# Optimization experiments

Hardware: AMD Instinct MI355X
Metric: run time of the kernel (lower is better)

Reference implementation:

```python
import jax, jax.numpy as jnp
import numpy as np

B, N, HID = 4, 16384, 512
H, M = 8, 32          # num_heads, num_slices
D = HID // H          # head_dim = 64


def setup_inputs() -> dict:
    key = jax.random.key(0)
    ks = jax.random.split(key, 8)
    std = 0.02
    return {
        "x": jax.random.normal(ks[0], (B, N, HID), jnp.float32),
        # Linear weights stored as [in, out] (y = x @ W + b)
        "wkv_w": jax.random.normal(ks[1], (HID, 2 * HID), jnp.float32) * std,
        "wkv_b": jnp.zeros((2 * HID,), jnp.float32),
        "wtq": jax.random.normal(ks[2], (H, M, D), jnp.float32) * std,
        "alpha": jnp.ones((H,), jnp.float32),
        "qkv_w": jax.random.normal(ks[3], (HID, 3 * HID), jnp.float32) * std,
        "out_w": jax.random.normal(ks[4], (HID, HID), jnp.float32) * std,
        "out_b": jnp.zeros((HID,), jnp.float32),
    }


def _split_heads(t):  # [b, n, h*d] -> [b, h, n, d]
    b, n, _ = t.shape
    return t.reshape(b, n, H, D).transpose(0, 2, 1, 3)


def _mha(q, k, v):
    scale = q.shape[-1] ** -0.5
    dots = jnp.einsum('bhqd,bhkd->bhqk', q, k) * scale
    attn = jax.nn.softmax(dots, axis=-1)
    out = jnp.einsum('bhqk,bhkd->bhqd', attn, v)
    return out, attn


def reference(x, wkv_w, wkv_b, wtq, alpha, qkv_w, out_w, out_b):
    kv = x @ wkv_w + wkv_b                      # [b, n, 2*hid]
    xk, xv = kv[..., :HID], kv[..., HID:]
    xk = _split_heads(xk)                       # [b, h, n, d]
    xv = _split_heads(xv)

    # slot/slice cross-attention: softmax over the slice axis m (axis=-2)
    slice_scores = jnp.einsum('hmd,bhnd->bhmn', wtq, xk)
    slice_weights = jax.nn.softmax(slice_scores * alpha[None, :, None, None], axis=-2)
    slice_token = jnp.einsum('bhmn,bhnd->bhmd', slice_weights, xv)
    slice_token = slice_token / (slice_weights.sum(axis=-1, keepdims=True) + 1e-5)
    slice_token = slice_token.transpose(0, 2, 1, 3).reshape(B, M, HID)  # b m (h d)

    # small inner MHA over the m=32 slices
    qkv = slice_token @ qkv_w                   # [b, m, 3*hid]
    q_t = _split_heads(qkv[..., :HID])
    k_t = _split_heads(qkv[..., HID:2 * HID])
    v_t = _split_heads(qkv[..., 2 * HID:])
    out_token, attn_weights = _mha(q_t, k_t, v_t)

    # scatter slice outputs back to n positions
    out = jnp.einsum('bhmd,bhmn->bhnd', out_token, slice_weights)
    out = out.transpose(0, 2, 1, 3).reshape(B, N, HID)  # b n (h d)
    out = out @ out_w + out_b
    return out, slice_weights, alpha, jnp.zeros((H, M), jnp.float32), attn_weights
```

## Files before the change

kernel.cpp:

```cpp
#include <hip/hip_runtime.h>

#define B_ 4
#define N_ 16384
#define HID_ 512
#define H_ 8
#define M_ 32
#define D_ 64

typedef __attribute__((ext_vector_type(8))) short short8;
typedef __attribute__((ext_vector_type(4))) float f32x4;

__device__ __forceinline__ short f2bf(float f) {
    unsigned u = __float_as_uint(f);
    u += 0x7fffu + ((u >> 16) & 1u);
    return (short)(u >> 16);
}
__device__ __forceinline__ float bf2f(short s) {
    return __uint_as_float(((unsigned)(unsigned short)s) << 16);
}
__device__ __forceinline__ unsigned pack2(float a, float b) {
    return (unsigned)(unsigned short)f2bf(a) | ((unsigned)(unsigned short)f2bf(b) << 16);
}
__device__ __forceinline__ void gl_lds16(const short* g, short* l) {
    __builtin_amdgcn_global_load_lds((const __attribute__((address_space(1))) unsigned*)g,
                                     (__attribute__((address_space(3))) unsigned*)l, 16, 0, 0);
}

__global__ void k_misc(const float* __restrict__ alpha, float* __restrict__ a_out,
                       float* __restrict__ z_out, const float* __restrict__ wtq,
                       short* __restrict__ wtq_bf) {
    int i = blockIdx.x * 256 + threadIdx.x;
    wtq_bf[i] = f2bf(wtq[i]);
    if (blockIdx.x == 0) {
        int t = threadIdx.x;
        if (t < H_) a_out[t] = alpha[t];
        z_out[t] = 0.f;
    }
}

__global__ void k_cvt(const float* __restrict__ src, short* __restrict__ dst) {
    int i = blockIdx.x * 256 + threadIdx.x;
    const f32x4* s = (const f32x4*)(src) + (size_t)i * 2;
    f32x4 a = s[0], b = s[1];
    short8 o;
    o[0] = f2bf(a[0]); o[1] = f2bf(a[1]); o[2] = f2bf(a[2]); o[3] = f2bf(a[3]);
    o[4] = f2bf(b[0]); o[5] = f2bf(b[1]); o[6] = f2bf(b[2]); o[7] = f2bf(b[3]);
    ((short8*)dst)[i] = o;
}

__global__ __launch_bounds__(256)
void k_wt(const float* __restrict__ w, short* __restrict__ wt) {
    __shared__ float ls[64][65];
    const int t = threadIdx.x;
    const int n0 = blockIdx.x * 64, k0 = blockIdx.y * 64;
#pragma unroll
    for (int p = 0; p < 16; ++p) {
        int idx = p * 256 + t;
        int kk = idx >> 6, nn = idx & 63;
        ls[kk][nn] = w[(size_t)(k0 + kk) * 1024 + n0 + nn];
    }
    __syncthreads();
#pragma unroll
    for (int p = 0; p < 16; ++p) {
        int idx = p * 256 + t;
        int nn = idx >> 6, kk = idx & 63;
        wt[(size_t)(n0 + nn) * 512 + k0 + kk] = f2bf(ls[kk][nn]);
    }
}

template <bool OUT_BF16>
__global__ __launch_bounds__(256, 2)
void mfma_gemm(const short* __restrict__ A, const short* __restrict__ Bt,
               const float* __restrict__ bias, void* __restrict__ Cv,
               int K, int Ncols, int b_stride, int rows_per_b, int lgx) {
    __shared__ short As[128 * 64];
    __shared__ short Bs[128 * 64];
    const int t = threadIdx.x;
    const int nwg = gridDim.x * gridDim.y;
    int id = blockIdx.y * gridDim.x + blockIdx.x;
    id = (id & 7) * (nwg >> 3) + (id >> 3);
    const int col0 = (id & ((1 << lgx) - 1)) * 128;
    const int row0 = (id >> lgx) * 128;
    const short* Bblk = Bt;
    if (b_stride) Bblk += (size_t)(row0 / rows_per_b) * (size_t)b_stride;

    int srow[4], scol[4];
#pragma unroll
    for (int c = 0; c < 4; ++c) {
        int lin = (c * 256 + t) * 16;
        int logo = lin ^ (((lin >> 7) & 7) << 4);
        srow[c] = logo >> 7;
        scol[c] = (logo & 127) >> 1;
    }

    const int w = t >> 6;
    const int L = t & 63;
    const int wm = (w >> 1) << 6;
    const int wn = (w & 1) << 6;
    const int lm = L & 15;
    const int lq = L >> 4;

    f32x4 acc[4][4];
#pragma unroll
    for (int i = 0; i < 4; ++i)
#pragma unroll
        for (int j = 0; j < 4; ++j) acc[i][j] = (f32x4){0.f, 0.f, 0.f, 0.f};

    for (int k0 = 0; k0 < K; k0 += 64) {
#pragma unroll
        for (int c = 0; c < 4; ++c) {
            gl_lds16(A + (size_t)(row0 + srow[c]) * K + k0 + scol[c], &As[(c * 256 + t) * 8]);
            gl_lds16(Bblk + (size_t)(col0 + srow[c]) * K + k0 + scol[c], &Bs[(c * 256 + t) * 8]);
        }
        __syncthreads();
#pragma unroll
        for (int ks = 0; ks < 2; ++ks) {
            short8 af[4], bfr[4];
#pragma unroll
            for (int i = 0; i < 4; ++i) {
                const int row = wm + (i << 4) + lm;
                int pb = (row << 7) + (ks << 6) + (lq << 4);
                pb ^= (row & 7) << 4;
                af[i] = *(const short8*)&As[pb >> 1];
            }
#pragma unroll
            for (int j = 0; j < 4; ++j) {
                const int row = wn + (j << 4) + lm;
                int pb = (row << 7) + (ks << 6) + (lq << 4);
                pb ^= (row & 7) << 4;
                bfr[j] = *(const short8*)&Bs[pb >> 1];
            }
#pragma unroll
            for (int i = 0; i < 4; ++i)
#pragma unroll
                for (int j = 0; j < 4; ++j)
                    acc[i][j] = __builtin_amdgcn_mfma_f32_16x16x32_bf16(af[i], bfr[j], acc[i][j], 0, 0, 0);
        }
        __syncthreads();
    }
#pragma unroll
    for (int i = 0; i < 4; ++i) {
#pragma unroll
        for (int j = 0; j < 4; ++j) {
            const int gr = row0 + wm + (i << 4) + (lq << 2);
            const int gc = col0 + wn + (j << 4) + lm;
            const float bv = bias[gc];
#pragma unroll
            for (int r = 0; r < 4; ++r) {
                float v = acc[i][j][r] + bv;
                if constexpr (OUT_BF16)
                    ((short*)Cv)[(size_t)(gr + r) * Ncols + gc] = f2bf(v);
                else
                    ((float*)Cv)[(size_t)(gr + r) * Ncols + gc] = v;
            }
        }
    }
}

__global__ __launch_bounds__(256, 4)
void k_score(const short* __restrict__ kv, const short* __restrict__ wtq_bf,
             const float* __restrict__ alpha, float* __restrict__ sw_out,
             short* __restrict__ swT, float* __restrict__ pws) {
    __shared__ __attribute__((aligned(16))) short wT_s[M_ * 256];
    const int t = threadIdx.x;
    const int bx = blockIdx.x;
    const int chunk = bx & 63;
    const int h = (bx >> 6) & 7;
    const int b = bx >> 9;
    const int w = t >> 6;
    const int L = t & 63;
    const int lm = L & 15;
    const int g = L >> 4;
    const int n0 = chunk * 256;
    const size_t rowb = (size_t)(b * N_ + n0);
    const float al = alpha[h];

    short8 bq[2][2];
    const short* wq = wtq_bf + h * (M_ * D_);
#pragma unroll
    for (int mt = 0; mt < 2; ++mt)
#pragma unroll
        for (int ks = 0; ks < 2; ++ks)
            bq[mt][ks] = *(const short8*)(wq + (mt * 16 + lm) * 64 + ks * 32 + g * 8);

    f32x4 s[4][2];
#pragma unroll
    for (int nt = 0; nt < 4; ++nt)
#pragma unroll
        for (int mt = 0; mt < 2; ++mt) s[nt][mt] = (f32x4){0.f, 0.f, 0.f, 0.f};
#pragma unroll
    for (int ks = 0; ks < 2; ++ks) {
        short8 aq[4];
#pragma unroll
        for (int nt = 0; nt < 4; ++nt)
            aq[nt] = *(const short8*)(kv + (rowb + w * 64 + nt * 16 + lm) * 1024 +
                                      h * 64 + ks * 32 + g * 8);
        __builtin_amdgcn_s_setprio(1);
#pragma unroll
        for (int nt = 0; nt < 4; ++nt)
#pragma unroll
            for (int mt = 0; mt < 2; ++mt)
                s[nt][mt] = __builtin_amdgcn_mfma_f32_16x16x32_bf16(aq[nt], bq[mt][ks], s[nt][mt], 0, 0, 0);
        __builtin_amdgcn_s_setprio(0);
    }

#pragma unroll
    for (int nt = 0; nt < 4; ++nt)
#pragma unroll
        for (int r = 0; r < 4; ++r) {
            float v0 = s[nt][0][r] * al, v1 = s[nt][1][r] * al;
            float mx = fmaxf(v0, v1);
#pragma unroll
            for (int d2 = 1; d2 < 16; d2 <<= 1) mx = fmaxf(mx, __shfl_xor(mx, d2));
            float e0 = __expf(v0 - mx), e1 = __expf(v1 - mx);
            float sm = e0 + e1;
#pragma unroll
            for (int d2 = 1; d2 < 16; d2 <<= 1) sm += __shfl_xor(sm, d2);
            float inv = 1.f / sm;
            s[nt][0][r] = e0 * inv;
            s[nt][1][r] = e1 * inv;
        }

    float ws0 = 0.f, ws1 = 0.f;
#pragma unroll
    for (int nt = 0; nt < 4; ++nt) {
        const int nn = w * 64 + nt * 16 + g * 4;
#pragma unroll
        for (int mt = 0; mt < 2; ++mt) {
            const int m = mt * 16 + lm;
            *(f32x4*)(sw_out + ((size_t)((b * 8 + h) * 32 + m)) * N_ + n0 + nn) = s[nt][mt];
            float w4 = s[nt][mt][0] + s[nt][mt][1] + s[nt][mt][2] + s[nt][mt][3];
            if (mt == 0) ws0 += w4; else ws1 += w4;
            unsigned lo = pack2(s[nt][mt][0], s[nt][mt][1]);
            unsigned hi = pack2(s[nt][mt][2], s[nt][mt][3]);
            *(uint2*)(wT_s + m * 256 + (nn ^ ((m & 7) << 3))) = make_uint2(lo, hi);
        }
    }
    ws0 += __shfl_xor(ws0, 16); ws0 += __shfl_xor(ws0, 32);
    ws1 += __shfl_xor(ws1, 16); ws1 += __shfl_xor(ws1, 32);
    if (L < 16) {
        float* pw = pws + (((size_t)((b * 8 + h) * 64 + chunk)) * 4 + w) * 32;
        pw[lm] = ws0;
        pw[16 + lm] = ws1;
    }
    __syncthreads();

    unsigned pk[16];
#pragma unroll
    for (int mp = 0; mp < 16; ++mp) {
        unsigned a0 = (unsigned short)wT_s[(2 * mp) * 256 + (t ^ (((2 * mp) & 7) << 3))];
        unsigned a1 = (unsigned short)wT_s[(2 * mp + 1) * 256 + (t ^ (((2 * mp + 1) & 7) << 3))];
        pk[mp] = a0 | (a1 << 16);
    }
    short8* swtp = (short8*)(swT + (rowb + t) * 256 + h * 32);
#pragma unroll
    for (int q = 0; q < 4; ++q) {
        short8 v;
        v[0] = (short)(pk[4 * q] & 0xffff);     v[1] = (short)(pk[4 * q] >> 16);
        v[2] = (short)(pk[4 * q + 1] & 0xffff); v[3] = (short)(pk[4 * q + 1] >> 16);
        v[4] = (short)(pk[4 * q + 2] & 0xffff); v[5] = (short)(pk[4 * q + 2] >> 16);
        v[6] = (short)(pk[4 * q + 3] & 0xffff); v[7] = (short)(pk[4 * q + 3] >> 16);
        swtp[q] = v;
    }
}

__global__ __attribute__((amdgpu_flat_work_group_size(256, 256), amdgpu_waves_per_eu(3, 3)))
void k_wsum(const short* __restrict__ kv, const short* __restrict__ swT,
            float* __restrict__ pnum) {
    __shared__ __attribute__((aligned(16))) short wT_s[M_ * 256];
    __shared__ __attribute__((aligned(16))) short xvT_s[D_ * 256];
    const int t = threadIdx.x;
    const int bx = blockIdx.x;
    const int chunk = bx & 63;
    const int h = (bx >> 6) & 7;
    const int b = bx >> 9;
    const int w = t >> 6;
    const int L = t & 63;
    const int lm = L & 15;
    const int g = L >> 4;
    const int n0 = chunk * 256;
    const size_t rowb = (size_t)(b * N_ + n0);

    short8 xv8[8];
    const short8* xvp = (const short8*)(kv + (rowb + t) * 1024 + HID_ + h * 64);
#pragma unroll
    for (int i = 0; i < 8; ++i) xv8[i] = xvp[i];

    short8 sw4[4];
    const short8* swp = (const short8*)(swT + (rowb + t) * 256 + h * 32);
#pragma unroll
    for (int q = 0; q < 4; ++q) sw4[q] = swp[q];

#pragma unroll
    for (int q = 0; q < 4; ++q)
#pragma unroll
        for (int j = 0; j < 8; ++j) {
            const int m = q * 8 + j;
            wT_s[m * 256 + (t ^ ((m & 7) << 3))] = sw4[q][j];
        }

#pragma unroll
    for (int i = 0; i < 8; ++i)
#pragma unroll
        for (int j = 0; j < 8; ++j)
            xvT_s[(i * 8 + j) * 256 + (t ^ (j << 3))] = xv8[i][j];

    __syncthreads();

    const int dcol = w * 16 + lm;
    f32x4 acc2[2];
    acc2[0] = (f32x4){0.f, 0.f, 0.f, 0.f};
    acc2[1] = (f32x4){0.f, 0.f, 0.f, 0.f};
#pragma unroll
    for (int ks = 0; ks < 8; ++ks) {
        const int kb = ks * 32 + g * 8;
        short8 bv = *(const short8*)(xvT_s + dcol * 256 + (kb ^ ((lm & 7) << 3)));
#pragma unroll
        for (int mt = 0; mt < 2; ++mt) {
            const int m = mt * 16 + lm;
            short8 av = *(const short8*)(wT_s + m * 256 + (kb ^ ((lm & 7) << 3)));
            acc2[mt] = __builtin_amdgcn_mfma_f32_16x16x32_bf16(av, bv, acc2[mt], 0, 0, 0);
        }
    }

    float* pn = pnum + ((size_t)((b * 8 + h) * 64 + chunk)) * 2048;
#pragma unroll
    for (int mt = 0; mt < 2; ++mt)
#pragma unroll
        for (int r = 0; r < 4; ++r)
            pn[(mt * 16 + g * 4 + r) * 64 + dcol] = acc2[mt][r];
}

__global__ __launch_bounds__(256)
void k_reduce(const float* __restrict__ pnum, const float* __restrict__ pws,
              float* __restrict__ num, float* __restrict__ wsum) {
    const int bid = blockIdx.x, t = threadIdx.x;
    if (bid < 256) {
        int e = bid * 256 + t;
        int bh = e >> 11, md = e & 2047;
        const float* p = pnum + (size_t)bh * 64 * 2048 + md;
        float s = 0.f;
#pragma unroll 4
        for (int c = 0; c < 64; ++c) s += p[c * 2048];
        num[e] = s;
    } else {
        int e = (bid - 256) * 256 + t;
        int bh = e >> 5, m = e & 31;
        const float* p = pws + (size_t)bh * 64 * 4 * 32 + m;
        float s = 0.f;
#pragma unroll 4
        for (int cw = 0; cw < 256; ++cw) s += p[cw * 32];
        wsum[e] = s;
    }
}

__global__ __launch_bounds__(256, 2)
void k_qkv(const float* __restrict__ num, const float* __restrict__ wsum,
           const float* __restrict__ qkv_w, float* __restrict__ qkv) {
    __shared__ float st_s[512 * 32];
    const int t = threadIdx.x;
    const int b = blockIdx.y;
    for (int p = 0; p < 64; ++p) {
        int idx = p * 256 + t;
        int m = idx & 31, k = idx >> 5;
        int h = k >> 6, d = k & 63;
        float wsv = wsum[(b * H_ + h) * M_ + m];
        st_s[k * 32 + m] = num[((size_t)(b * H_ + h) * M_ + m) * 64 + d] / (wsv + 1e-5f);
    }
    __syncthreads();
    const int m = t >> 3;
    const int c0 = blockIdx.x * 64 + (t & 7) * 8;
    float acc[8] = {};
    for (int k = 0; k < 512; ++k) {
        float sv = st_s[k * 32 + m];
        const f32x4* wp = (const f32x4*)(qkv_w + (size_t)k * 1536 + c0);
        f32x4 w0 = wp[0], w1 = wp[1];
        acc[0] += sv * w0[0]; acc[1] += sv * w0[1]; acc[2] += sv * w0[2]; acc[3] += sv * w0[3];
        acc[4] += sv * w1[0]; acc[5] += sv * w1[1]; acc[6] += sv * w1[2]; acc[7] += sv * w1[3];
    }
    float* dst = qkv + (size_t)(b * M_ + m) * 1536 + c0;
#pragma unroll
    for (int i = 0; i < 8; ++i) dst[i] = acc[i];
}

__global__ __launch_bounds__(256)
void k_mha(const float* __restrict__ qkv, float* __restrict__ attn_out,
           float* __restrict__ ot) {
    __shared__ float q_s[32 * 65], k_s[32 * 65], v_s[32 * 65];
    __shared__ float s_s[32 * 33], p_s[32 * 33];
    const int bx = blockIdx.x;
    const int b = bx >> 3, h = bx & 7;
    const int t = threadIdx.x;
    for (int p = 0; p < 8; ++p) {
        int idx = p * 256 + t;
        int m = idx >> 6, d = idx & 63;
        size_t base = (size_t)(b * M_ + m) * 1536 + h * 64 + d;
        q_s[m * 65 + d] = qkv[base];
        k_s[m * 65 + d] = qkv[base + 512];
        v_s[m * 65 + d] = qkv[base + 1024];
    }
    __syncthreads();
    for (int p = 0; p < 4; ++p) {
        int c = p * 256 + t;
        int m = c >> 5, mm = c & 31;
        float a = 0.f;
#pragma unroll
        for (int d = 0; d < 64; ++d) a += q_s[m * 65 + d] * k_s[mm * 65 + d];
        s_s[m * 33 + mm] = a * 0.125f;
    }
    __syncthreads();
    if (t < 32) {
        float mx = -1e30f;
        for (int mm = 0; mm < 32; ++mm) mx = fmaxf(mx, s_s[t * 33 + mm]);
        float sum = 0.f;
        for (int mm = 0; mm < 32; ++mm) {
            float e = __expf(s_s[t * 33 + mm] - mx);
            p_s[t * 33 + mm] = e;
            sum += e;
        }
        float inv = 1.f / sum;
        for (int mm = 0; mm < 32; ++mm) {
            float av = p_s[t * 33 + mm] * inv;
            p_s[t * 33 + mm] = av;
            attn_out[((size_t)(b * H_ + h) * M_ + t) * M_ + mm] = av;
        }
    }
    __syncthreads();
    const int m = t >> 3, d0 = (t & 7) * 8;
    float acc[8] = {};
    for (int mm = 0; mm < 32; ++mm) {
        float av = p_s[m * 33 + mm];
#pragma unroll
        for (int j = 0; j < 8; ++j) acc[j] += av * v_s[mm * 65 + d0 + j];
    }
    float* dst = ot + ((size_t)(b * H_ + h) * M_ + m) * 64 + d0;
#pragma unroll
    for (int j = 0; j < 8; ++j) dst[j] = acc[j];
}

__global__ __launch_bounds__(256)
void k_p(const float* __restrict__ ot, const float* __restrict__ out_w,
         short* __restrict__ Pt) {
    __shared__ float ot_s[32 * 65];
    const int bh = blockIdx.y;
    const int b = bh >> 3, h = bh & 7;
    const int t = threadIdx.x;
    for (int p = 0; p < 8; ++p) {
        int idx = p * 256 + t;
        int m = idx >> 6, d = idx & 63;
        ot_s[m * 65 + d] = ot[(size_t)bh * (M_ * 64) + idx];
    }
    __syncthreads();
    const int j = blockIdx.x * 128 + (t & 127);
    const int mh = (t >> 7) * 16;
    float acc[16] = {};
    for (int d = 0; d < 64; ++d) {
        float ow = out_w[(size_t)(h * 64 + d) * HID_ + j];
#pragma unroll
        for (int i = 0; i < 16; ++i) acc[i] += ot_s[(mh + i) * 65 + d] * ow;
    }
    short* dst = Pt + ((size_t)b * HID_ + j) * (H_ * M_) + h * M_ + mh;
#pragma unroll
    for (int i = 0; i < 16; i += 2) *(unsigned*)(dst + i) = pack2(acc[i], acc[i + 1]);
}

extern "C" void kernel_launch(void* const* d_in, const int* in_sizes, int n_in,
                              void* d_out, int out_size, void* d_ws, size_t ws_size,
                              hipStream_t stream) {
    const float* x     = (const float*)d_in[0];
    const float* wkv_w = (const float*)d_in[1];
    const float* wkv_b = (const float*)d_in[2];
    const float* wtq   = (const float*)d_in[3];
    const float* alpha = (const float*)d_in[4];
    const float* qkv_w = (const float*)d_in[5];
    const float* out_w = (const float*)d_in[6];
    const float* out_b = (const float*)d_in[7];

    float* out       = (float*)d_out;
    float* sw_out    = out + (size_t)B_ * N_ * HID_;
    float* alpha_out = sw_out + (size_t)B_ * H_ * M_ * N_;
    float* zeros_out = alpha_out + H_;
    float* attn_out  = zeros_out + H_ * M_;

    short* x_bf = (short*)sw_out;
    float* pnum = out;
    float* pws  = out + 4194304;

    char* ws = (char*)d_ws;
    short* kv   = (short*)(ws);
    short* swT  = (short*)(ws + 134217728);
    short* wkvT = (short*)(ws + 167772160);
    short* Pt   = (short*)(ws + 168820736);
    float* num  = (float*)(ws + 169869312);
    float* wsum = (float*)(ws + 170131456);
    float* qkvb = (float*)(ws + 170135552);
    float* ot   = (float*)(ws + 170921984);
    short* wtq_bf = (short*)(ws + 170921984);

    k_misc<<<64, 256, 0, stream>>>(alpha, alpha_out, zeros_out, wtq, wtq_bf);
    k_cvt<<<16384, 256, 0, stream>>>(x, x_bf);
    k_wt<<<dim3(16, 8), 256, 0, stream>>>(wkv_w, wkvT);
    mfma_gemm<true><<<dim3(8, 512), 256, 0, stream>>>(
        x_bf, wkvT, wkv_b, (void*)kv, 512, 1024, 0, 1 << 30, 3);
    k_score<<<2048, 256, 0, stream>>>(kv, wtq_bf, alpha, sw_out, swT, pws);
    k_wsum<<<2048, 256, 0, stream>>>(kv, swT, pnum);
    k_reduce<<<260, 256, 0, stream>>>(pnum, pws, num, wsum);
    k_qkv<<<dim3(24, 4), 256, 0, stream>>>(num, wsum, qkv_w, qkvb);
    k_mha<<<32, 256, 0, stream>>>(qkvb, attn_out, ot);
    k_p<<<dim3(4, 32), 256, 0, stream>>>(ot, out_w, Pt);
    mfma_gemm<false><<<dim3(4, 512), 256, 0, stream>>>(
        swT, Pt, out_b, (void*)out, 256, 512, 131072, 16384, 2);
}
```

Before: 551.6 us.

## Fold slice-query weights into K projection and compute scores directly from x

Precomputes an effective weight Weff = Wk_h · wtq_h (plus an effective bias) so slice scores come from a single x @ Weff GEMM with K=512 and 256 outputs. The full 1024-wide KV projection becomes a V-only 512-wide projection, so the K half is never materialized. The change removes GEMM FLOPs and halves the kv intermediate's write and read traffic. In exchange, scores are computed from bf16 x against a bf16-rounded fused weight, which changes rounding, and a new score GEMM kernel with a softmax epilogue is added.

```diff
diff --git a/kernel.cpp b/kernel.cpp
--- a/kernel.cpp
+++ b/kernel.cpp
@@ -27,15 +27,10 @@
 }
 
 __global__ void k_misc(const float* __restrict__ alpha, float* __restrict__ a_out,
-                       float* __restrict__ z_out, const float* __restrict__ wtq,
-                       short* __restrict__ wtq_bf) {
-    int i = blockIdx.x * 256 + threadIdx.x;
-    wtq_bf[i] = f2bf(wtq[i]);
-    if (blockIdx.x == 0) {
-        int t = threadIdx.x;
-        if (t < H_) a_out[t] = alpha[t];
-        z_out[t] = 0.f;
-    }
+                       float* __restrict__ z_out) {
+    int t = threadIdx.x;
+    if (t < H_) a_out[t] = alpha[t];
+    z_out[t] = 0.f;
 }
 
 __global__ void k_cvt(const float* __restrict__ src, short* __restrict__ dst) {
@@ -52,7 +47,7 @@
 void k_wt(const float* __restrict__ w, short* __restrict__ wt) {
     __shared__ float ls[64][65];
     const int t = threadIdx.x;
-    const int n0 = blockIdx.x * 64, k0 = blockIdx.y * 64;
+    const int n0 = (blockIdx.x + 8) * 64, k0 = blockIdx.y * 64;
 #pragma unroll
     for (int p = 0; p < 16; ++p) {
         int idx = p * 256 + t;
@@ -65,6 +60,32 @@
         int idx = p * 256 + t;
         int nn = idx >> 6, kk = idx & 63;
         wt[(size_t)(n0 + nn) * 512 + k0 + kk] = f2bf(ls[kk][nn]);
+    }
+}
+
+__global__ __launch_bounds__(256)
+void k_weff(const float* __restrict__ wkv_w, const float* __restrict__ wkv_b,
+            const float* __restrict__ wtq, short* __restrict__ WeffT,
+            float* __restrict__ beff) {
+    __shared__ float wq_s[64];
+    const int c = blockIdx.x;
+    const int h = c >> 5;
+    const int t = threadIdx.x;
+    if (t < 64) wq_s[t] = wtq[c * 64 + t];
+    __syncthreads();
+#pragma unroll
+    for (int kk = 0; kk < 2; ++kk) {
+        const int k = kk * 256 + t;
+        const float* wr = wkv_w + (size_t)k * 1024 + h * 64;
+        float a = 0.f;
+#pragma unroll
+        for (int d = 0; d < 64; ++d) a += wr[d] * wq_s[d];
+        WeffT[c * 512 + k] = f2bf(a);
+    }
+    if (t == 0) {
+        float a = 0.f;
+        for (int d = 0; d < 64; ++d) a += wkv_b[h * 64 + d] * wq_s[d];
+        beff[c] = a;
     }
 }
 
@@ -157,11 +178,158 @@
     }
 }
 
-__global__ __launch_bounds__(256, 4)
-void k_score(const short* __restrict__ kv, const short* __restrict__ wtq_bf,
-             const float* __restrict__ alpha, float* __restrict__ sw_out,
-             short* __restrict__ swT, float* __restrict__ pws) {
+__global__ __launch_bounds__(256, 2)
+void k_scoreg(const short* __restrict__ A, const short* __restrict__ WeffT,
+              const float* __restrict__ beff, const float* __restrict__ alpha,
+              float* __restrict__ sw_out, short* __restrict__ swT,
+              float* __restrict__ pws) {
+    __shared__ __attribute__((aligned(16))) short smem[16384];
+    short* As = smem;
+    short* Bs = smem + 8192;
+    short* wT_s = smem;
+    const int t = threadIdx.x;
+    int id = blockIdx.y * 2 + blockIdx.x;
+    id = (id & 7) * 128 + (id >> 3);
+    const int xc = id & 1;
+    const int row0 = (id >> 1) * 128;
+    const int col0 = xc * 128;
+    const int K = 512;
+
+    int srow[4], scol[4];
+#pragma unroll
+    for (int c = 0; c < 4; ++c) {
+        int lin = (c * 256 + t) * 16;
+        int logo = lin ^ (((lin >> 7) & 7) << 4);
+        srow[c] = logo >> 7;
+        scol[c] = (logo & 127) >> 1;
+    }
+    const int w = t >> 6;
+    const int L = t & 63;
+    const int wm = (w >> 1) << 6;
+    const int wn = (w & 1) << 6;
+    const int lm = L & 15;
+    const int lq = L >> 4;
+
+    f32x4 acc[4][4];
+#pragma unroll
+    for (int i = 0; i < 4; ++i)
+#pragma unroll
+        for (int j = 0; j < 4; ++j) acc[i][j] = (f32x4){0.f, 0.f, 0.f, 0.f};
+
+    for (int k0 = 0; k0 < K; k0 += 64) {
+#pragma unroll
+        for (int c = 0; c < 4; ++c) {
+            gl_lds16(A + (size_t)(row0 + srow[c]) * K + k0 + scol[c], &As[(c * 256 + t) * 8]);
+            gl_lds16(WeffT + (size_t)(col0 + srow[c]) * K + k0 + scol[c], &Bs[(c * 256 + t) * 8]);
+        }
+        __syncthreads();
+#pragma unroll
+        for (int ks = 0; ks < 2; ++ks) {
+            short8 af[4], bfr[4];
+#pragma unroll
+            for (int i = 0; i < 4; ++i) {
+                const int row = wm + (i << 4) + lm;
+                int pb = (row << 7) + (ks << 6) + (lq << 4);
+                pb ^= (row & 7) << 4;
+                af[i] = *(const short8*)&As[pb >> 1];
+            }
+#pragma unroll
+            for (int j = 0; j < 4; ++j) {
+                const int row = wn + (j << 4) + lm;
+                int pb = (row << 7) + (ks << 6) + (lq << 4);
+                pb ^= (row & 7) << 4;
+                bfr[j] = *(const short8*)&Bs[pb >> 1];
+            }
+#pragma unroll
+            for (int i = 0; i < 4; ++i)
+#pragma unroll
+                for (int j = 0; j < 4; ++j)
+                    acc[i][j] = __builtin_amdgcn_mfma_f32_16x16x32_bf16(af[i], bfr[j], acc[i][j], 0, 0, 0);
+        }
+        __syncthreads();
+    }
+
+    const int b = row0 >> 14;
+    const int nb = row0 & 16383;
+    float be[4], alf[2];
+#pragma unroll
+    for (int j = 0; j < 4; ++j) be[j] = beff[col0 + wn + (j << 4) + lm];
+#pragma unroll
+    for (int hh = 0; hh < 2; ++hh) alf[hh] = alpha[xc * 4 + (w & 1) * 2 + hh];
+
+#pragma unroll
+    for (int i = 0; i < 4; ++i)
+#pragma unroll
+        for (int r = 0; r < 4; ++r)
+#pragma unroll
+            for (int hh = 0; hh < 2; ++hh) {
+                float v0 = (acc[i][2 * hh][r] + be[2 * hh]) * alf[hh];
+                float v1 = (acc[i][2 * hh + 1][r] + be[2 * hh + 1]) * alf[hh];
+                float mx = fmaxf(v0, v1);
+#pragma unroll
+                for (int d2 = 1; d2 < 16; d2 <<= 1) mx = fmaxf(mx, __shfl_xor(mx, d2));
+                float e0 = __expf(v0 - mx), e1 = __expf(v1 - mx);
+                float sm = e0 + e1;
+#pragma unroll
+                for (int d2 = 1; d2 < 16; d2 <<= 1) sm += __shfl_xor(sm, d2);
+                float inv = 1.f / sm;
+                acc[i][2 * hh][r] = e0 * inv;
+                acc[i][2 * hh + 1][r] = e1 * inv;
+            }
+
+    float wsj[4] = {0.f, 0.f, 0.f, 0.f};
+#pragma unroll
+    for (int i = 0; i < 4; ++i) {
+        const int tokb = wm + (i << 4) + (lq << 2);
+#pragma unroll
+        for (int j = 0; j < 4; ++j) {
+            const int h = xc * 4 + (w & 1) * 2 + (j >> 1);
+            const int m = ((j & 1) << 4) + lm;
+            f32x4 vv = acc[i][j];
+            *(f32x4*)(sw_out + ((size_t)((b * 8 + h) * 32 + m)) * N_ + nb + tokb) = vv;
+            wsj[j] += vv[0] + vv[1] + vv[2] + vv[3];
+            const int c = wn + (j << 4) + lm;
+            unsigned lo = pack2(vv[0], vv[1]);
+            unsigned hi = pack2(vv[2], vv[3]);
+            *(uint2*)(wT_s + c * 128 + (tokb ^ ((c & 7) << 3))) = make_uint2(lo, hi);
+        }
+    }
+#pragma unroll
+    for (int j = 0; j < 4; ++j) {
+        wsj[j] += __shfl_xor(wsj[j], 16);
+        wsj[j] += __shfl_xor(wsj[j], 32);
+    }
+    if (L < 16) {
+        const int panel = nb >> 7;
+#pragma unroll
+        for (int hh = 0; hh < 2; ++hh) {
+            const int h = xc * 4 + (w & 1) * 2 + hh;
+            float* pw = pws + (((size_t)((b * 8 + h) * 128 + panel)) * 2 + (w >> 1)) * 32;
+            pw[lm] = wsj[2 * hh];
+            pw[16 + lm] = wsj[2 * hh + 1];
+        }
+    }
+    __syncthreads();
+
+    const int tok = t & 127, ch = t >> 7;
+    short8* swtp = (short8*)(swT + ((size_t)(b * N_ + nb + tok)) * 256 + xc * 128 + ch * 64);
+#pragma unroll
+    for (int q = 0; q < 8; ++q) {
+        short8 v;
+#pragma unroll
+        for (int e = 0; e < 8; ++e) {
+            const int c = ch * 64 + q * 8 + e;
+            v[e] = wT_s[c * 128 + (tok ^ ((c & 7) << 3))];
+        }
+        swtp[q] = v;
+    }
+}
+
+__global__ __attribute__((amdgpu_flat_work_group_size(256, 256), amdgpu_waves_per_eu(3, 3)))
+void k_wsum(const short* __restrict__ v, const short* __restrict__ swT,
+            float* __restrict__ pnum) {
     __shared__ __attribute__((aligned(16))) short wT_s[M_ * 256];
+    __shared__ __attribute__((aligned(16))) short xvT_s[D_ * 256];
     const int t = threadIdx.x;
     const int bx = blockIdx.x;
     const int chunk = bx & 63;
@@ -173,116 +341,9 @@
     const int g = L >> 4;
     const int n0 = chunk * 256;
     const size_t rowb = (size_t)(b * N_ + n0);
-    const float al = alpha[h];
-
-    short8 bq[2][2];
-    const short* wq = wtq_bf + h * (M_ * D_);
-#pragma unroll
-    for (int mt = 0; mt < 2; ++mt)
-#pragma unroll
-        for (int ks = 0; ks < 2; ++ks)
-            bq[mt][ks] = *(const short8*)(wq + (mt * 16 + lm) * 64 + ks * 32 + g * 8);
-
-    f32x4 s[4][2];
-#pragma unroll
-    for (int nt = 0; nt < 4; ++nt)
-#pragma unroll
-        for (int mt = 0; mt < 2; ++mt) s[nt][mt] = (f32x4){0.f, 0.f, 0.f, 0.f};
-#pragma unroll
-    for (int ks = 0; ks < 2; ++ks) {
-        short8 aq[4];
-#pragma unroll
-        for (int nt = 0; nt < 4; ++nt)
-            aq[nt] = *(const short8*)(kv + (rowb + w * 64 + nt * 16 + lm) * 1024 +
-                                      h * 64 + ks * 32 + g * 8);
-        __builtin_amdgcn_s_setprio(1);
-#pragma unroll
-        for (int nt = 0; nt < 4; ++nt)
-#pragma unroll
-            for (int mt = 0; mt < 2; ++mt)
-                s[nt][mt] = __builtin_amdgcn_mfma_f32_16x16x32_bf16(aq[nt], bq[mt][ks], s[nt][mt], 0, 0, 0);
-        __builtin_amdgcn_s_setprio(0);
-    }
-
-#pragma unroll
-    for (int nt = 0; nt < 4; ++nt)
-#pragma unroll
-        for (int r = 0; r < 4; ++r) {
-            float v0 = s[nt][0][r] * al, v1 = s[nt][1][r] * al;
-            float mx = fmaxf(v0, v1);
-#pragma unroll
-            for (int d2 = 1; d2 < 16; d2 <<= 1) mx = fmaxf(mx, __shfl_xor(mx, d2));
-            float e0 = __expf(v0 - mx), e1 = __expf(v1 - mx);
-            float sm = e0 + e1;
-#pragma unroll
-            for (int d2 = 1; d2 < 16; d2 <<= 1) sm += __shfl_xor(sm, d2);
-            float inv = 1.f / sm;
-            s[nt][0][r] = e0 * inv;
-            s[nt][1][r] = e1 * inv;
-        }
-
-    float ws0 = 0.f, ws1 = 0.f;
-#pragma unroll
-    for (int nt = 0; nt < 4; ++nt) {
-        const int nn = w * 64 + nt * 16 + g * 4;
-#pragma unroll
-        for (int mt = 0; mt < 2; ++mt) {
-            const int m = mt * 16 + lm;
-            *(f32x4*)(sw_out + ((size_t)((b * 8 + h) * 32 + m)) * N_ + n0 + nn) = s[nt][mt];
-            float w4 = s[nt][mt][0] + s[nt][mt][1] + s[nt][mt][2] + s[nt][mt][3];
-            if (mt == 0) ws0 += w4; else ws1 += w4;
-            unsigned lo = pack2(s[nt][mt][0], s[nt][mt][1]);
-            unsigned hi = pack2(s[nt][mt][2], s[nt][mt][3]);
-            *(uint2*)(wT_s + m * 256 + (nn ^ ((m & 7) << 3))) = make_uint2(lo, hi);
-        }
-    }
-    ws0 += __shfl_xor(ws0, 16); ws0 += __shfl_xor(ws0, 32);
-    ws1 += __shfl_xor(ws1, 16); ws1 += __shfl_xor(ws1, 32);
-    if (L < 16) {
-        float* pw = pws + (((size_t)((b * 8 + h) * 64 + chunk)) * 4 + w) * 32;
-        pw[lm] = ws0;
-        pw[16 + lm] = ws1;
-    }
-    __syncthreads();
-
-    unsigned pk[16];
-#pragma unroll
-    for (int mp = 0; mp < 16; ++mp) {
-        unsigned a0 = (unsigned short)wT_s[(2 * mp) * 256 + (t ^ (((2 * mp) & 7) << 3))];
-        unsigned a1 = (unsigned short)wT_s[(2 * mp + 1) * 256 + (t ^ (((2 * mp + 1) & 7) << 3))];
-        pk[mp] = a0 | (a1 << 16);
-    }
-    short8* swtp = (short8*)(swT + (rowb + t) * 256 + h * 32);
-#pragma unroll
-    for (int q = 0; q < 4; ++q) {
-        short8 v;
-        v[0] = (short)(pk[4 * q] & 0xffff);     v[1] = (short)(pk[4 * q] >> 16);
-        v[2] = (short)(pk[4 * q + 1] & 0xffff); v[3] = (short)(pk[4 * q + 1] >> 16);
-        v[4] = (short)(pk[4 * q + 2] & 0xffff); v[5] = (short)(pk[4 * q + 2] >> 16);
-        v[6] = (short)(pk[4 * q + 3] & 0xffff); v[7] = (short)(pk[4 * q + 3] >> 16);
-        swtp[q] = v;
-    }
-}
-
-__global__ __attribute__((amdgpu_flat_work_group_size(256, 256), amdgpu_waves_per_eu(3, 3)))
-void k_wsum(const short* __restrict__ kv, const short* __restrict__ swT,
-            float* __restrict__ pnum) {
-    __shared__ __attribute__((aligned(16))) short wT_s[M_ * 256];
-    __shared__ __attribute__((aligned(16))) short xvT_s[D_ * 256];
-    const int t = threadIdx.x;
-    const int bx = blockIdx.x;
-    const int chunk = bx & 63;
-    const int h = (bx >> 6) & 7;
-    const int b = bx >> 9;
-    const int w = t >> 6;
-    const int L = t & 63;
-    const int lm = L & 15;
-    const int g = L >> 4;
-    const int n0 = chunk * 256;
-    const size_t rowb = (size_t)(b * N_ + n0);
 
     short8 xv8[8];
-    const short8* xvp = (const short8*)(kv + (rowb + t) * 1024 + HID_ + h * 64);
+    const short8* xvp = (const short8*)(v + (rowb + t) * 512 + h * 64);
 #pragma unroll
     for (int i = 0; i < 8; ++i) xv8[i] = xvp[i];
 
@@ -346,7 +407,7 @@
     } else {
         int e = (bid - 256) * 256 + t;
         int bh = e >> 5, m = e & 31;
-        const float* p = pws + (size_t)bh * 64 * 4 * 32 + m;
+        const float* p = pws + (size_t)bh * 8192 + m;
         float s = 0.f;
 #pragma unroll 4
         for (int cw = 0; cw < 256; ++cw) s += p[cw * 32];
@@ -482,12 +543,12 @@
     float* zeros_out = alpha_out + H_;
     float* attn_out  = zeros_out + H_ * M_;
 
-    short* x_bf = (short*)sw_out;
     float* pnum = out;
     float* pws  = out + 4194304;
 
     char* ws = (char*)d_ws;
-    short* kv   = (short*)(ws);
+    short* v    = (short*)(ws);
+    short* x_bf = (short*)(ws + 67108864);
     short* swT  = (short*)(ws + 134217728);
     short* wkvT = (short*)(ws + 167772160);
     short* Pt   = (short*)(ws + 168820736);
@@ -495,15 +556,18 @@
     float* wsum = (float*)(ws + 170131456);
     float* qkvb = (float*)(ws + 170135552);
     float* ot   = (float*)(ws + 170921984);
-    short* wtq_bf = (short*)(ws + 170921984);
-
-    k_misc<<<64, 256, 0, stream>>>(alpha, alpha_out, zeros_out, wtq, wtq_bf);
+    short* WeffT = (short*)(ws + 170921984);
+    float* beff  = (float*)(ws + 170131456);
+
+    k_misc<<<1, 256, 0, stream>>>(alpha, alpha_out, zeros_out);
     k_cvt<<<16384, 256, 0, stream>>>(x, x_bf);
-    k_wt<<<dim3(16, 8), 256, 0, stream>>>(wkv_w, wkvT);
-    mfma_gemm<true><<<dim3(8, 512), 256, 0, stream>>>(
-        x_bf, wkvT, wkv_b, (void*)kv, 512, 1024, 0, 1 << 30, 3);
-    k_score<<<2048, 256, 0, stream>>>(kv, wtq_bf, alpha, sw_out, swT, pws);
-    k_wsum<<<2048, 256, 0, stream>>>(kv, swT, pnum);
+    k_wt<<<dim3(8, 8), 256, 0, stream>>>(wkv_w, wkvT);
+    k_weff<<<256, 256, 0, stream>>>(wkv_w, wkv_b, wtq, WeffT, beff);
+    mfma_gemm<true><<<dim3(4, 512), 256, 0, stream>>>(
+        x_bf, wkvT + 512 * 512, wkv_b + 512, (void*)v, 512, 512, 0, 1 << 30, 2);
+    k_scoreg<<<dim3(2, 512), 256, 0, stream>>>(
+        x_bf, WeffT, beff, alpha, sw_out, swT, pws);
+    k_wsum<<<2048, 256, 0, stream>>>(v, swT, pnum);
     k_reduce<<<260, 256, 0, stream>>>(pnum, pws, num, wsum);
     k_qkv<<<dim3(24, 4), 256, 0, stream>>>(num, wsum, qkv_w, qkvb);
     k_mha<<<32, 256, 0, stream>>>(qkvb, attn_out, ot);
```

Result: faster. 533.7 us (-3.2%).
